# Performance work log

Hardware: AMD Instinct MI355X
Metric: run time of the kernel (lower is better)

Reference implementation:

```python
import jax, jax.numpy as jnp
import numpy as np

BATCH = 8192
NUM_VARS = 128
HID = 64
NUM_PARAMS = 2


def setup_inputs() -> dict:
    key = jax.random.key(0)
    ks = jax.random.split(key, 7)
    s = 0.1  # keep activations in a sane range
    return {
        "x": jax.random.normal(ks[0], (BATCH, NUM_VARS), jnp.float32),
        "w0": jax.random.normal(ks[1], (NUM_VARS, HID, NUM_VARS), jnp.float32) * s,
        "b0": jax.random.normal(ks[2], (NUM_VARS, HID), jnp.float32) * s,
        "w1": jax.random.normal(ks[3], (NUM_VARS, HID, HID), jnp.float32) * s,
        "b1": jax.random.normal(ks[4], (NUM_VARS, HID), jnp.float32) * s,
        "w2": jax.random.normal(ks[5], (NUM_VARS, NUM_PARAMS, HID), jnp.float32) * s,
        "b2": jax.random.normal(ks[6], (NUM_VARS, NUM_PARAMS), jnp.float32) * s,
    }


def reference(x, w0, b0, w1, b1, w2, b2):
    # adjacency = ones - eye (no self-loops), constant buffer in the torch model
    d = x.shape[1]
    adj = jnp.ones((d, d), x.dtype) - jnp.eye(d, dtype=x.dtype)  # [j, t]
    # layer 0: per-node masked linear over all other variables
    # torch: einsum('tij,ljt,bj->bti', w0, adj[None], x) + b0
    h = jnp.einsum('tij,jt,bj->bti', w0, adj, x) + b0  # [B, t=num_vars, hid]
    h = jax.nn.leaky_relu(h)  # negative_slope=0.01, matches F.leaky_relu
    # layer 1: per-node linear
    h = jnp.einsum('tij,btj->bti', w1, h) + b1
    h = jax.nn.leaky_relu(h)
    # output layer (no activation)
    out = jnp.einsum('tij,btj->bti', w2, h) + b2  # [B, num_vars, num_params]
    # torch returns torch.unbind(out, 1); we return the stacked equivalent
    return out
```

## Files before the change

kernel.cpp:

```cpp
#include <hip/hip_runtime.h>
#include <hip/hip_bf16.h>

typedef __attribute__((ext_vector_type(8))) short short8;
typedef __attribute__((ext_vector_type(16))) float f32x16;

#define LEAK 0.01f

__device__ __forceinline__ f32x16 mfma32(short8 a, short8 b, f32x16 c) {
    return __builtin_amdgcn_mfma_f32_32x32x16_bf16(a, b, c, 0, 0, 0);
}
__device__ __forceinline__ unsigned pkbf(float a, float b) {
    __hip_bfloat162 t = __float22bfloat162_rn(make_float2(a, b));
    return *reinterpret_cast<unsigned*>(&t);
}
__device__ __forceinline__ void plswap(unsigned &a, unsigned &b, int h) {
    unsigned ax = (unsigned)__shfl_xor((int)a, 32);
    unsigned bx = (unsigned)__shfl_xor((int)b, 32);
    unsigned na = h ? bx : a;
    unsigned nb = h ? b  : ax;
    a = na; b = nb;
}

__device__ __forceinline__ void transition(const f32x16 &A0, const f32x16 &A1,
                                           short8 out[4], int h) {
    unsigned pk[2][8];
    #pragma unroll
    for (int nt = 0; nt < 2; ++nt) {
        const f32x16 &A = nt ? A1 : A0;
        #pragma unroll
        for (int s = 0; s < 8; ++s) {
            float u = A[2*s], v = A[2*s+1];
            u = fmaxf(u, LEAK * u); v = fmaxf(v, LEAK * v);
            pk[nt][s] = pkbf(u, v);
        }
    }
    #pragma unroll
    for (int ks = 0; ks < 4; ++ks) {
        const int nt = ks >> 1, ss = (ks & 1) * 4;
        unsigned d0 = pk[nt][ss], d1 = pk[nt][ss+1], d2 = pk[nt][ss+2], d3 = pk[nt][ss+3];
        plswap(d0, d2, h);
        plswap(d1, d3, h);
        union { unsigned u[4]; short8 s; } U;
        U.u[0] = d0; U.u[1] = d1; U.u[2] = d2; U.u[3] = d3;
        out[ks] = U.s;
    }
}

__global__ __launch_bounds__(256) void prep_kernel(
    const float* __restrict__ x,  const float* __restrict__ w0, const float* __restrict__ b0,
    const float* __restrict__ w1, const float* __restrict__ b1,
    const float* __restrict__ w2, const float* __restrict__ b2,
    __hip_bfloat16* __restrict__ xp,  __hip_bfloat16* __restrict__ w0p,
    __hip_bfloat16* __restrict__ w1p, __hip_bfloat16* __restrict__ w2p)
{
    const int idx = blockIdx.x * 256 + threadIdx.x;
    float v[8];
    #pragma unroll
    for (int e = 0; e < 8; ++e) v[e] = 0.f;
    __hip_bfloat16* dst;

    if (idx < 147456) {
        int b = idx / 18, ch = idx - b * 18;
        dst = xp + b * 144 + ch * 8;
        if (ch < 16) {
            const float* s = x + b * 128 + ch * 8;
            #pragma unroll
            for (int e = 0; e < 8; ++e) v[e] = s[e];
        } else if (ch == 16) v[0] = 1.f;
    } else if (idx < 294912) {
        int i = idx - 147456;
        int r = i / 18, ch = i - r * 18;
        int t = r >> 6;
        dst = w0p + r * 144 + ch * 8;
        if (ch < 16) {
            const float* s = w0 + r * 128 + ch * 8;
            #pragma unroll
            for (int e = 0; e < 8; ++e) v[e] = s[e];
            if ((t >> 3) == ch) v[t & 7] = 0.f;
        } else if (ch == 16) v[0] = b0[r];
    } else if (idx < 376832) {
        int i = idx - 294912;
        int r = i / 10, ch = i - r * 10;
        dst = w1p + r * 80 + ch * 8;
        if (ch < 8) {
            const float* s = w1 + r * 64 + ch * 8;
            #pragma unroll
            for (int e = 0; e < 8; ++e) v[e] = s[e];
        } else if (ch == 8) v[0] = b1[r];
    } else {
        int i = idx - 376832;
        int r = i / 10, ch = i - r * 10;
        int t = r >> 5, n = r & 31;
        dst = w2p + r * 80 + ch * 8;
        if (n < 2) {
            if (ch < 8) {
                const float* s = w2 + (t * 2 + n) * 64 + ch * 8;
                #pragma unroll
                for (int e = 0; e < 8; ++e) v[e] = s[e];
            } else if (ch == 8) v[0] = b2[t * 2 + n];
        }
    }
    union { unsigned u[4]; short8 s; } U;
    #pragma unroll
    for (int p = 0; p < 4; ++p) U.u[p] = pkbf(v[2*p], v[2*p+1]);
    *reinterpret_cast<short8*>(dst) = U.s;
}

__global__ __launch_bounds__(256, 2) void mlp_kernel(
    const __hip_bfloat16* __restrict__ xp,
    const __hip_bfloat16* __restrict__ w0p,
    const __hip_bfloat16* __restrict__ w1p,
    const __hip_bfloat16* __restrict__ w2p,
    float* __restrict__ dst, int direct)
{
    const int tid  = threadIdx.x;
    const int wave = tid >> 6;
    const int lane = tid & 63;
    const int h    = lane >> 5;
    const int c    = lane & 31;

    const int bid   = blockIdx.x;
    const int t     = (bid & 7) * 16 + ((bid >> 3) & 15);
    const int chunk = bid >> 7;
    const int rb0   = chunk * 1024 + wave * 256;

    const __hip_bfloat16* w0t = w0p + t * 9216;
    const __hip_bfloat16* w1t = w1p + t * 5120;
    const __hip_bfloat16* w2t = w2p + t * 2560;
    short8 w0f[2][9], w1f[2][5], w2f[5];
    #pragma unroll
    for (int nt = 0; nt < 2; ++nt)
        #pragma unroll
        for (int ks = 0; ks < 9; ++ks)
            w0f[nt][ks] = *reinterpret_cast<const short8*>(w0t + (nt*32 + c)*144 + ks*16 + h*8);
    #pragma unroll
    for (int nt = 0; nt < 2; ++nt)
        #pragma unroll
        for (int ks = 0; ks < 5; ++ks)
            w1f[nt][ks] = *reinterpret_cast<const short8*>(w1t + (nt*32 + c)*80 + ks*16 + h*8);
    #pragma unroll
    for (int ks = 0; ks < 5; ++ks)
        w2f[ks] = *reinterpret_cast<const short8*>(w2t + c*80 + ks*16 + h*8);

    union { unsigned u[4]; short8 s; } OneU;
    OneU.u[0] = (h == 0) ? 0x00003f80u : 0u;
    OneU.u[1] = 0u; OneU.u[2] = 0u; OneU.u[3] = 0u;
    const short8 onef = OneU.s;

    #pragma unroll 1
    for (int tile = 0; tile < 8; ++tile) {
        const int brow = rb0 + tile * 32 + c;
        const __hip_bfloat16* xr = xp + brow * 144 + h * 8;
        short8 xf[9];
        #pragma unroll
        for (int ks = 0; ks < 9; ++ks)
            xf[ks] = *reinterpret_cast<const short8*>(xr + ks * 16);

        f32x16 acc0a, acc0b;
        #pragma unroll
        for (int i = 0; i < 16; ++i) { acc0a[i] = 0.f; acc0b[i] = 0.f; }
        #pragma unroll
        for (int ks = 0; ks < 9; ++ks) acc0a = mfma32(w0f[0][ks], xf[ks], acc0a);
        #pragma unroll
        for (int ks = 0; ks < 9; ++ks) acc0b = mfma32(w0f[1][ks], xf[ks], acc0b);

        short8 h1f[4];
        transition(acc0a, acc0b, h1f, h);

        f32x16 acc1a, acc1b;
        #pragma unroll
        for (int i = 0; i < 16; ++i) { acc1a[i] = 0.f; acc1b[i] = 0.f; }
        #pragma unroll
        for (int ks = 0; ks < 4; ++ks) acc1a = mfma32(w1f[0][ks], h1f[ks], acc1a);
        acc1a = mfma32(w1f[0][4], onef, acc1a);
        #pragma unroll
        for (int ks = 0; ks < 4; ++ks) acc1b = mfma32(w1f[1][ks], h1f[ks], acc1b);
        acc1b = mfma32(w1f[1][4], onef, acc1b);

        short8 h2f[4];
        transition(acc1a, acc1b, h2f, h);

        f32x16 acc2;
        #pragma unroll
        for (int i = 0; i < 16; ++i) acc2[i] = 0.f;
        #pragma unroll
        for (int ks = 0; ks < 4; ++ks) acc2 = mfma32(w2f[ks], h2f[ks], acc2);
        acc2 = mfma32(w2f[4], onef, acc2);

        if (h == 0) {
            float2 v = make_float2(acc2[0], acc2[1]);
            if (direct) *reinterpret_cast<float2*>(dst + brow * 256 + t * 2) = v;
            else        *reinterpret_cast<float2*>(dst + t * 16384 + brow * 2) = v;
        }
    }
}

__global__ __launch_bounds__(256) void transpose_kernel(
    const float* __restrict__ tmp, float* __restrict__ out)
{
    __shared__ float tile[32][257];
    const int b0 = blockIdx.x * 32;
    const int tid = threadIdx.x;
    #pragma unroll
    for (int it = 0; it < 16; ++it) {
        int idx = it * 256 + tid;
        int tt = idx >> 5, r = idx & 31;
        float2 v = *reinterpret_cast<const float2*>(tmp + tt * 16384 + (b0 + r) * 2);
        tile[r][tt * 2]     = v.x;
        tile[r][tt * 2 + 1] = v.y;
    }
    __syncthreads();
    #pragma unroll
    for (int r = 0; r < 32; ++r)
        out[(b0 + r) * 256 + tid] = tile[r][tid];
}

extern "C" void kernel_launch(void* const* d_in, const int* in_sizes, int n_in,
                              void* d_out, int out_size, void* d_ws, size_t ws_size,
                              hipStream_t stream)
{
    const float* x  = (const float*)d_in[0];
    const float* w0 = (const float*)d_in[1];
    const float* b0 = (const float*)d_in[2];
    const float* w1 = (const float*)d_in[3];
    const float* b1 = (const float*)d_in[4];
    const float* w2 = (const float*)d_in[5];
    const float* b2 = (const float*)d_in[6];
    float* out = (float*)d_out;

    const size_t OFF_W0  = 2359296;
    const size_t OFF_W1  = OFF_W0 + 2359296;
    const size_t OFF_W2  = OFF_W1 + 1310720;
    const size_t OFF_TMP = OFF_W2 + 655360;
    const size_t NEED_TMP = OFF_TMP + 8388608;

    if (ws_size < OFF_TMP) return;

    char* ws = (char*)d_ws;
    __hip_bfloat16* xp  = (__hip_bfloat16*)(ws);
    __hip_bfloat16* w0p = (__hip_bfloat16*)(ws + OFF_W0);
    __hip_bfloat16* w1p = (__hip_bfloat16*)(ws + OFF_W1);
    __hip_bfloat16* w2p = (__hip_bfloat16*)(ws + OFF_W2);
    float* tmp = (float*)(ws + OFF_TMP);

    const int use_tmp = (ws_size >= NEED_TMP) ? 1 : 0;
    float* dstp = use_tmp ? tmp : out;

    prep_kernel<<<1632, 256, 0, stream>>>(x, w0, b0, w1, b1, w2, b2, xp, w0p, w1p, w2p);
    mlp_kernel<<<1024, 256, 0, stream>>>(xp, w0p, w1p, w2p, dstp, use_tmp ? 0 : 1);
    if (use_tmp)
        transpose_kernel<<<256, 256, 0, stream>>>(tmp, out);
}
```

Baseline: 129.4 us.

## Prefetch next x tile, interleave MFMA chains, use permlane32 swap and setprio

Each wave now loads the x fragments for the next 32-row tile while the current tile's MFMAs run, so global load latency overlaps with compute. The two independent accumulator chains are interleaved so back-to-back MFMAs have no dependency. MFMA sections are wrapped in s_setprio to favour the math-issuing wave. The cross-half swap uses the permlane32_swap builtin when it is available, replacing two shuffles and selects. The costs are higher register pressure from the extra xn buffer and the unroll of 2, which could cut occupancy under the 2-blocks launch bound.

```diff
diff --git a/kernel.cpp b/kernel.cpp
--- a/kernel.cpp
+++ b/kernel.cpp
@@ -3,6 +3,7 @@
 
 typedef __attribute__((ext_vector_type(8))) short short8;
 typedef __attribute__((ext_vector_type(16))) float f32x16;
+typedef __attribute__((ext_vector_type(2))) unsigned uint2v;
 
 #define LEAK 0.01f
 
@@ -13,6 +14,13 @@
     __hip_bfloat162 t = __float22bfloat162_rn(make_float2(a, b));
     return *reinterpret_cast<unsigned*>(&t);
 }
+
+#if defined(__has_builtin) && __has_builtin(__builtin_amdgcn_permlane32_swap)
+__device__ __forceinline__ void plswap(unsigned &a, unsigned &b, int ) {
+    uint2v r = __builtin_amdgcn_permlane32_swap(a, b, false, false);
+    a = r.x; b = r.y;
+}
+#else
 __device__ __forceinline__ void plswap(unsigned &a, unsigned &b, int h) {
     unsigned ax = (unsigned)__shfl_xor((int)a, 32);
     unsigned bx = (unsigned)__shfl_xor((int)b, 32);
@@ -20,6 +28,7 @@
     unsigned nb = h ? b  : ax;
     a = na; b = nb;
 }
+#endif
 
 __device__ __forceinline__ void transition(const f32x16 &A0, const f32x16 &A1,
                                            short8 out[4], int h) {
@@ -124,6 +133,12 @@
     const int chunk = bid >> 7;
     const int rb0   = chunk * 1024 + wave * 256;
 
+    const __hip_bfloat16* xr0 = xp + (rb0 + c) * 144 + h * 8;
+    short8 xf[9];
+    #pragma unroll
+    for (int ks = 0; ks < 9; ++ks)
+        xf[ks] = *reinterpret_cast<const short8*>(xr0 + ks * 16);
+
     const __hip_bfloat16* w0t = w0p + t * 9216;
     const __hip_bfloat16* w1t = w1p + t * 5120;
     const __hip_bfloat16* w2t = w2p + t * 2560;
@@ -147,22 +162,28 @@
     OneU.u[1] = 0u; OneU.u[2] = 0u; OneU.u[3] = 0u;
     const short8 onef = OneU.s;
 
-    #pragma unroll 1
+    #pragma unroll 2
     for (int tile = 0; tile < 8; ++tile) {
         const int brow = rb0 + tile * 32 + c;
-        const __hip_bfloat16* xr = xp + brow * 144 + h * 8;
-        short8 xf[9];
-        #pragma unroll
-        for (int ks = 0; ks < 9; ++ks)
-            xf[ks] = *reinterpret_cast<const short8*>(xr + ks * 16);
+
+        short8 xn[9];
+        if (tile < 7) {
+            const __hip_bfloat16* xr = xr0 + (tile + 1) * (32 * 144);
+            #pragma unroll
+            for (int ks = 0; ks < 9; ++ks)
+                xn[ks] = *reinterpret_cast<const short8*>(xr + ks * 16);
+        }
 
         f32x16 acc0a, acc0b;
         #pragma unroll
         for (int i = 0; i < 16; ++i) { acc0a[i] = 0.f; acc0b[i] = 0.f; }
-        #pragma unroll
-        for (int ks = 0; ks < 9; ++ks) acc0a = mfma32(w0f[0][ks], xf[ks], acc0a);
-        #pragma unroll
-        for (int ks = 0; ks < 9; ++ks) acc0b = mfma32(w0f[1][ks], xf[ks], acc0b);
+        __builtin_amdgcn_s_setprio(1);
+        #pragma unroll
+        for (int ks = 0; ks < 9; ++ks) {
+            acc0a = mfma32(w0f[0][ks], xf[ks], acc0a);
+            acc0b = mfma32(w0f[1][ks], xf[ks], acc0b);
+        }
+        __builtin_amdgcn_s_setprio(0);
 
         short8 h1f[4];
         transition(acc0a, acc0b, h1f, h);
@@ -170,12 +191,15 @@
         f32x16 acc1a, acc1b;
         #pragma unroll
         for (int i = 0; i < 16; ++i) { acc1a[i] = 0.f; acc1b[i] = 0.f; }
-        #pragma unroll
-        for (int ks = 0; ks < 4; ++ks) acc1a = mfma32(w1f[0][ks], h1f[ks], acc1a);
+        __builtin_amdgcn_s_setprio(1);
+        #pragma unroll
+        for (int ks = 0; ks < 4; ++ks) {
+            acc1a = mfma32(w1f[0][ks], h1f[ks], acc1a);
+            acc1b = mfma32(w1f[1][ks], h1f[ks], acc1b);
+        }
         acc1a = mfma32(w1f[0][4], onef, acc1a);
-        #pragma unroll
-        for (int ks = 0; ks < 4; ++ks) acc1b = mfma32(w1f[1][ks], h1f[ks], acc1b);
         acc1b = mfma32(w1f[1][4], onef, acc1b);
+        __builtin_amdgcn_s_setprio(0);
 
         short8 h2f[4];
         transition(acc1a, acc1b, h2f, h);
@@ -183,15 +207,20 @@
         f32x16 acc2;
         #pragma unroll
         for (int i = 0; i < 16; ++i) acc2[i] = 0.f;
+        __builtin_amdgcn_s_setprio(1);
         #pragma unroll
         for (int ks = 0; ks < 4; ++ks) acc2 = mfma32(w2f[ks], h2f[ks], acc2);
         acc2 = mfma32(w2f[4], onef, acc2);
+        __builtin_amdgcn_s_setprio(0);
 
         if (h == 0) {
             float2 v = make_float2(acc2[0], acc2[1]);
             if (direct) *reinterpret_cast<float2*>(dst + brow * 256 + t * 2) = v;
             else        *reinterpret_cast<float2*>(dst + t * 16384 + brow * 2) = v;
         }
+
+        #pragma unroll
+        for (int ks = 0; ks < 9; ++ks) xf[ks] = xn[ks];
     }
 }
 
```

After: 120.2 us. -7.1%, faster.
